# Optimization experiments

Hardware: AMD Instinct MI355X
Metric: run time of the kernel (lower is better)

Reference implementation:

```python
import jax, jax.numpy as jnp
import numpy as np

N, E, IN, ED, H, C, G, NC = 50000, 800000, 128, 32, 4, 16, 64, 2
HC = H * C  # 64
NEG_SLOPE = 0.2
EPS = 1e-5


def _layernorm(x, g, b):
    mu = jnp.mean(x, axis=-1, keepdims=True)
    var = jnp.mean((x - mu) ** 2, axis=-1, keepdims=True)
    return (x - mu) * jax.lax.rsqrt(var + EPS) * g + b


def _gat(x, src, dst, edge_attr, W, a_src, a_dst, We, a_edge, b):
    """PyG GATConv (v1) with edge features, concat=True."""
    n = x.shape[0]
    h, c = a_src.shape
    xw = (x @ W).reshape(n, h, c)                       # [N,H,C]
    al_src = jnp.sum(xw * a_src, axis=-1)               # [N,H]
    al_dst = jnp.sum(xw * a_dst, axis=-1)               # [N,H]
    ew = (edge_attr @ We).reshape(-1, h, c)             # [Ef,H,C]
    al_e = jnp.sum(ew * a_edge, axis=-1)                # [Ef,H]
    alpha = al_src[src] + al_dst[dst] + al_e            # [Ef,H]
    alpha = jnp.where(alpha > 0, alpha, NEG_SLOPE * alpha)
    # segment softmax over incoming edges of each dst node
    amax = jax.ops.segment_max(alpha, dst, num_segments=n)
    amax = jnp.where(jnp.isfinite(amax), amax, 0.0)
    ex = jnp.exp(alpha - amax[dst])
    denom = jax.ops.segment_sum(ex, dst, num_segments=n)
    att = ex / (denom[dst] + 1e-16)                     # [Ef,H]
    msg = xw[src] * att[:, :, None]                     # [Ef,H,C]
    out = jax.ops.segment_sum(msg, dst, num_segments=n) # [N,H,C]
    return out.reshape(n, h * c) + b


def setup_inputs() -> dict:
    ks = jax.random.split(jax.random.key(0), 24)
    s = 0.1
    inp = {
        "x": jax.random.normal(ks[0], (N, IN), jnp.float32),
        "edge_attr": jax.random.normal(ks[1], (E, ED), jnp.float32),
        "W1": jax.random.normal(ks[2], (IN, HC), jnp.float32) * s,
        "as1": jax.random.normal(ks[3], (H, C), jnp.float32) * s,
        "ad1": jax.random.normal(ks[4], (H, C), jnp.float32) * s,
        "We1": jax.random.normal(ks[5], (ED, HC), jnp.float32) * s,
        "ae1": jax.random.normal(ks[6], (H, C), jnp.float32) * s,
        "b1": jnp.zeros((HC,), jnp.float32),
        "W2": jax.random.normal(ks[7], (HC, HC), jnp.float32) * s,
        "as2": jax.random.normal(ks[8], (H, C), jnp.float32) * s,
        "ad2": jax.random.normal(ks[9], (H, C), jnp.float32) * s,
        "We2": jax.random.normal(ks[10], (ED, HC), jnp.float32) * s,
        "ae2": jax.random.normal(ks[11], (H, C), jnp.float32) * s,
        "b2": jnp.zeros((HC,), jnp.float32),
        "g1": jnp.ones((HC,), jnp.float32),
        "be1": jnp.zeros((HC,), jnp.float32),
        "fw1": jax.random.normal(ks[12], (HC, 32), jnp.float32) * s,
        "fb1": jnp.zeros((32,), jnp.float32),
        "g2": jnp.ones((32,), jnp.float32),
        "be2": jnp.zeros((32,), jnp.float32),
        "fw2": jax.random.normal(ks[13], (32, NC), jnp.float32) * s,
        "fb2": jnp.zeros((NC,), jnp.float32),
        "edge_index": jax.random.randint(ks[14], (2, E), 0, N, jnp.int64),
        "batch": jnp.sort(jax.random.randint(ks[15], (N,), 0, G, jnp.int64)),
    }
    return inp


def reference(x, edge_attr, W1, as1, ad1, We1, ae1, b1, W2, as2, ad2, We2, ae2,
              b2, g1, be1, fw1, fb1, g2, be2, fw2, fb2, edge_index, batch):
    src, dst = edge_index[0], edge_index[1]
    e = edge_attr.shape[0]
    # add_self_loops with fill_value='mean' (mean of incoming edge_attr per node)
    cnt = jax.ops.segment_sum(jnp.ones((e,), x.dtype), dst, num_segments=N)
    loop_ea = jax.ops.segment_sum(edge_attr, dst, num_segments=N) / jnp.clip(cnt, 1.0)[:, None]
    ar = jnp.arange(N)
    src_f = jnp.concatenate([src, ar])
    dst_f = jnp.concatenate([dst, ar])
    ea_f = jnp.concatenate([edge_attr, loop_ea], axis=0)

    h = _gat(x, src_f, dst_f, ea_f, W1, as1, ad1, We1, ae1, b1)
    h = jax.nn.relu(h)
    h = _layernorm(h, g1, be1)
    h = _gat(h, src_f, dst_f, ea_f, W2, as2, ad2, We2, ae2, b2)
    h = jax.nn.relu(h)
    pooled = jax.ops.segment_max(h, batch, num_segments=G)   # global_max_pool
    pooled = jnp.where(jnp.isfinite(pooled), pooled, 0.0)
    z = pooled @ fw1 + fb1
    z = _layernorm(z, g2, be2)
    z = jax.nn.relu(z)
    # dropout(p=0.4) is identity in eval mode
    z = z @ fw2 + fb2
    return jax.nn.log_softmax(z, axis=1)
```

## Files before the change

kernel.cpp:

```cpp
#include <hip/hip_runtime.h>
#include <math.h>

#define N_NODES 50000
#define N_EDGES 800000
#define IN_DIM 128
#define ED_DIM 32
#define NH 4
#define CH 16
#define HC 64
#define NG 64
#define NCL 2
#define NEG_SLOPE 0.2f
#define LN_EPS 1e-5f
#define NBLK1 196
#define NB_TILE 3125
#define NB_ECH 3125

__global__ void k_scan_local(const int* __restrict__ cnt, int* __restrict__ tmp_ex,
                             int* __restrict__ bsum) {
    __shared__ int sd[256];
    int t = threadIdx.x, idx = blockIdx.x * 256 + t;
    int v = (idx < N_NODES) ? cnt[idx] : 0;
    sd[t] = v; __syncthreads();
    for (int off = 1; off < 256; off <<= 1) {
        int add = (t >= off) ? sd[t - off] : 0;
        __syncthreads();
        sd[t] += add;
        __syncthreads();
    }
    if (idx < N_NODES) tmp_ex[idx] = sd[t] - v;
    if (t == 255) bsum[blockIdx.x] = sd[t];
}

__global__ __launch_bounds__(256) void k_phase1(
        const float* __restrict__ X, const float* __restrict__ W,
        const float* __restrict__ AS, const float* __restrict__ AD,
        float* __restrict__ XW, float* __restrict__ ALS, float* __restrict__ ALD,
        const float* __restrict__ ea,
        const float* __restrict__ We1, const float* __restrict__ ae1,
        const float* __restrict__ We2, const float* __restrict__ ae2,
        float4* __restrict__ ale8,
        const int* __restrict__ dst, int* __restrict__ cnt, int* __restrict__ rank_e) {
    __shared__ float smem[IN_DIM * HC + 16 * IN_DIM];
    int job = blockIdx.x % 3;
    int bid = blockIdx.x / 3;
    int t = threadIdx.x;
    if (job == 0) {
        const int K = IN_DIM;
        float* sW = smem;
        float* sX = smem + K * HC;
        for (int i = t; i < K * HC; i += 256) sW[i] = W[i];
        int nb = bid * 16;
        for (int i = t; i < 16 * K; i += 256) sX[i] = X[(long long)nb * K + i];
        __syncthreads();
        int sub = t >> 6, j = t & 63;
        float acc[4] = {0.f, 0.f, 0.f, 0.f};
        #pragma unroll 8
        for (int k = 0; k < K; ++k) {
            float wv = sW[k * HC + j];
            #pragma unroll
            for (int q = 0; q < 4; ++q) acc[q] += sX[(sub + 4 * q) * K + k] * wv;
        }
        float as_ = AS[j], ad_ = AD[j];
        #pragma unroll
        for (int q = 0; q < 4; ++q) {
            int n = nb + sub + 4 * q;
            XW[(long long)n * HC + j] = acc[q];
            float vs = acc[q] * as_, vd = acc[q] * ad_;
            #pragma unroll
            for (int m = 1; m < 16; m <<= 1) { vs += __shfl_xor(vs, m); vd += __shfl_xor(vd, m); }
            if ((j & 15) == 0) {
                int h = j >> 4;
                ALS[n * 4 + h] = vs; ALD[n * 4 + h] = vd;
            }
        }
    } else if (job == 1) {
        float* sVe = smem;
        {
            int d = t >> 3, k = t & 7;
            int l = k >> 2, h = k & 3;
            const float* We = l ? We2 : We1;
            const float* ae = l ? ae2 : ae1;
            float s = 0.f;
            #pragma unroll
            for (int c = 0; c < CH; ++c) s += We[d * HC + h * CH + c] * ae[h * CH + c];
            sVe[d * 8 + k] = s;
        }
        __syncthreads();
        int e = bid * 256 + t;
        if (e >= N_EDGES) return;
        float a[8];
        #pragma unroll
        for (int k = 0; k < 8; ++k) a[k] = 0.f;
        const float4* er4 = (const float4*)(ea + (long long)e * ED_DIM);
        #pragma unroll
        for (int q = 0; q < ED_DIM / 4; ++q) {
            float4 v = er4[q];
            float ev[4] = {v.x, v.y, v.z, v.w};
            #pragma unroll
            for (int u = 0; u < 4; ++u) {
                #pragma unroll
                for (int k = 0; k < 8; ++k) a[k] += ev[u] * sVe[(q * 4 + u) * 8 + k];
            }
        }
        float4* out = ale8 + (long long)e * 2;
        out[0] = make_float4(a[0], a[1], a[2], a[3]);
        out[1] = make_float4(a[4], a[5], a[6], a[7]);
    } else {
        int e = bid * 256 + t;
        if (e < N_EDGES) rank_e[e] = atomicAdd(&cnt[dst[e]], 1);
    }
}

__global__ void k_scan_perm(const int* __restrict__ tmp_ex, const int* __restrict__ bsum,
                            int* __restrict__ row_start,
                            const int* __restrict__ dst, const int* __restrict__ srcI,
                            const int* __restrict__ rank_e, int2* __restrict__ perm_src) {
    __shared__ int sd[256];
    __shared__ int sboff[256];
    int t = threadIdx.x;
    int v = (t < NBLK1) ? bsum[t] : 0;
    sd[t] = v; __syncthreads();
    for (int off = 1; off < 256; off <<= 1) {
        int add = (t >= off) ? sd[t - off] : 0;
        __syncthreads();
        sd[t] += add;
        __syncthreads();
    }
    sboff[t] = sd[t] - v;
    __syncthreads();
    if (blockIdx.x < NBLK1) {
        int idx = blockIdx.x * 256 + t;
        if (idx < N_NODES) row_start[idx] = tmp_ex[idx] + sboff[blockIdx.x];
        if (idx == 0) row_start[N_NODES] = N_EDGES;
    } else {
        int e = (blockIdx.x - NBLK1) * 256 + t;
        if (e < N_EDGES) {
            int d = dst[e];
            int pos = tmp_ex[d] + sboff[d >> 8] + rank_e[e];
            perm_src[pos] = make_int2(e, srcI[e]);
        }
    }
}

__global__ void k_agg1x(const int* __restrict__ rs, const int2* __restrict__ ps,
                        const float* __restrict__ ale8,
                        const float* __restrict__ ALS, const float* __restrict__ ALD,
                        const float* __restrict__ XW, const float* __restrict__ bias,
                        const float* __restrict__ gam, const float* __restrict__ bet,
                        const float* __restrict__ W2,
                        const float* __restrict__ AS2, const float* __restrict__ AD2,
                        float* __restrict__ XW2, float* __restrict__ ALS2,
                        float* __restrict__ ALD2) {
    __shared__ float sh[4][HC];
    int wid = threadIdx.x >> 6;
    int n = (blockIdx.x * blockDim.x + threadIdx.x) >> 6;
    if (n >= N_NODES) return;
    int lane = threadIdx.x & 63;
    int h = lane >> 4;
    int e0 = rs[n], e1 = rs[n + 1];
    float adn = ALD[n * 4 + h];
    float acc0 = 0.f, l0 = 0.f, as0 = 0.f;
    float acc1 = 0.f, l1 = 0.f, as1 = 0.f;
    float acc2 = 0.f, l2 = 0.f, as2 = 0.f;
    float acc3 = 0.f, l3 = 0.f, as3 = 0.f;
    int e = e0;
    for (; e + 3 < e1; e += 4) {
        int2 pA = ps[e], pB = ps[e + 1], pC = ps[e + 2], pD = ps[e + 3];
        float aeA = ale8[(long long)pA.x * 8 + h];
        float aeB = ale8[(long long)pB.x * 8 + h];
        float aeC = ale8[(long long)pC.x * 8 + h];
        float aeD = ale8[(long long)pD.x * 8 + h];
        float xA = XW[pA.y * HC + lane];
        float xB = XW[pB.y * HC + lane];
        float xC = XW[pC.y * HC + lane];
        float xD = XW[pD.y * HC + lane];
        float aA = ALS[pA.y * 4 + h] + adn + aeA;
        float aB = ALS[pB.y * 4 + h] + adn + aeB;
        float aC = ALS[pC.y * 4 + h] + adn + aeC;
        float aD = ALS[pD.y * 4 + h] + adn + aeD;
        aA = aA > 0.f ? aA : NEG_SLOPE * aA;
        aB = aB > 0.f ? aB : NEG_SLOPE * aB;
        aC = aC > 0.f ? aC : NEG_SLOPE * aC;
        aD = aD > 0.f ? aD : NEG_SLOPE * aD;
        float qA = __expf(aA), qB = __expf(aB), qC = __expf(aC), qD = __expf(aD);
        acc0 += qA * xA; l0 += qA; as0 += aeA;
        acc1 += qB * xB; l1 += qB; as1 += aeB;
        acc2 += qC * xC; l2 += qC; as2 += aeC;
        acc3 += qD * xD; l3 += qD; as3 += aeD;
    }
    for (; e < e1; ++e) {
        int2 pA = ps[e];
        float aeA = ale8[(long long)pA.x * 8 + h];
        float xA = XW[pA.y * HC + lane];
        float aA = ALS[pA.y * 4 + h] + adn + aeA;
        aA = aA > 0.f ? aA : NEG_SLOPE * aA;
        float qA = __expf(aA);
        acc0 += qA * xA; l0 += qA; as0 += aeA;
    }
    int d = e1 - e0;
    float invd = 1.f / (float)(d > 0 ? d : 1);
    float aSelf = ALS[n * 4 + h] + adn + (as0 + as1 + as2 + as3) * invd;
    aSelf = aSelf > 0.f ? aSelf : NEG_SLOPE * aSelf;
    float pS = __expf(aSelf);
    float acc = (acc0 + acc1) + (acc2 + acc3) + pS * XW[n * HC + lane];
    float l = (l0 + l1) + (l2 + l3) + pS;
    float v = acc / (l + 1e-16f) + bias[lane];
    v = fmaxf(v, 0.f);
    {
        float s1 = v;
        #pragma unroll
        for (int mm = 1; mm < 64; mm <<= 1) s1 += __shfl_xor(s1, mm);
        float mean = s1 * (1.f / 64.f);
        float dd = v - mean;
        float s2 = dd * dd;
        #pragma unroll
        for (int mm = 1; mm < 64; mm <<= 1) s2 += __shfl_xor(s2, mm);
        float var = s2 * (1.f / 64.f);
        v = dd * rsqrtf(var + LN_EPS) * gam[lane] + bet[lane];
    }
    sh[wid][lane] = v;
    __syncthreads();
    float a2 = 0.f;
    #pragma unroll 8
    for (int k = 0; k < HC; ++k) {
        a2 += sh[wid][k] * W2[k * HC + lane];
    }
    XW2[(long long)n * HC + lane] = a2;
    float vs = a2 * AS2[lane], vd = a2 * AD2[lane];
    #pragma unroll
    for (int m = 1; m < 16; m <<= 1) { vs += __shfl_xor(vs, m); vd += __shfl_xor(vd, m); }
    if ((lane & 15) == 0) {
        ALS2[n * 4 + h] = vs; ALD2[n * 4 + h] = vd;
    }
}

__global__ void k_agg2p(const int* __restrict__ rs, const int2* __restrict__ ps,
                        const float* __restrict__ ale8,
                        const float* __restrict__ ALS, const float* __restrict__ ALD,
                        const float* __restrict__ XW, const float* __restrict__ bias,
                        const int* __restrict__ batch, float* __restrict__ pooled) {
    int n = (blockIdx.x * blockDim.x + threadIdx.x) >> 6;
    if (n >= N_NODES) return;
    int lane = threadIdx.x & 63;
    int h = lane >> 4;
    int e0 = rs[n], e1 = rs[n + 1];
    float adn = ALD[n * 4 + h];
    float acc0 = 0.f, l0 = 0.f, as0 = 0.f;
    float acc1 = 0.f, l1 = 0.f, as1 = 0.f;
    float acc2 = 0.f, l2 = 0.f, as2 = 0.f;
    float acc3 = 0.f, l3 = 0.f, as3 = 0.f;
    int e = e0;
    for (; e + 3 < e1; e += 4) {
        int2 pA = ps[e], pB = ps[e + 1], pC = ps[e + 2], pD = ps[e + 3];
        float aeA = ale8[(long long)pA.x * 8 + 4 + h];
        float aeB = ale8[(long long)pB.x * 8 + 4 + h];
        float aeC = ale8[(long long)pC.x * 8 + 4 + h];
        float aeD = ale8[(long long)pD.x * 8 + 4 + h];
        float xA = XW[pA.y * HC + lane];
        float xB = XW[pB.y * HC + lane];
        float xC = XW[pC.y * HC + lane];
        float xD = XW[pD.y * HC + lane];
        float aA = ALS[pA.y * 4 + h] + adn + aeA;
        float aB = ALS[pB.y * 4 + h] + adn + aeB;
        float aC = ALS[pC.y * 4 + h] + adn + aeC;
        float aD = ALS[pD.y * 4 + h] + adn + aeD;
        aA = aA > 0.f ? aA : NEG_SLOPE * aA;
        aB = aB > 0.f ? aB : NEG_SLOPE * aB;
        aC = aC > 0.f ? aC : NEG_SLOPE * aC;
        aD = aD > 0.f ? aD : NEG_SLOPE * aD;
        float qA = __expf(aA), qB = __expf(aB), qC = __expf(aC), qD = __expf(aD);
        acc0 += qA * xA; l0 += qA; as0 += aeA;
        acc1 += qB * xB; l1 += qB; as1 += aeB;
        acc2 += qC * xC; l2 += qC; as2 += aeC;
        acc3 += qD * xD; l3 += qD; as3 += aeD;
    }
    for (; e < e1; ++e) {
        int2 pA = ps[e];
        float aeA = ale8[(long long)pA.x * 8 + 4 + h];
        float xA = XW[pA.y * HC + lane];
        float aA = ALS[pA.y * 4 + h] + adn + aeA;
        aA = aA > 0.f ? aA : NEG_SLOPE * aA;
        float qA = __expf(aA);
        acc0 += qA * xA; l0 += qA; as0 += aeA;
    }
    int d = e1 - e0;
    float invd = 1.f / (float)(d > 0 ? d : 1);
    float aSelf = ALS[n * 4 + h] + adn + (as0 + as1 + as2 + as3) * invd;
    aSelf = aSelf > 0.f ? aSelf : NEG_SLOPE * aSelf;
    float pS = __expf(aSelf);
    float acc = (acc0 + acc1) + (acc2 + acc3) + pS * XW[n * HC + lane];
    float l = (l0 + l1) + (l2 + l3) + pS;
    float v = acc / (l + 1e-16f) + bias[lane];
    v = fmaxf(v, 0.f);
    int g = batch[n];
    atomicMax((unsigned int*)&pooled[g * HC + lane], __float_as_uint(v));
}

__global__ void k_head(const float* __restrict__ pooled,
                       const float* __restrict__ fw1, const float* __restrict__ fb1,
                       const float* __restrict__ g2, const float* __restrict__ be2,
                       const float* __restrict__ fw2, const float* __restrict__ fb2,
                       float* __restrict__ out) {
    int g = blockIdx.x;
    int j = threadIdx.x;
    float z = 0.f;
    if (j < 32) {
        for (int k = 0; k < HC; ++k) z += pooled[g * HC + k] * fw1[k * 32 + j];
        z += fb1[j];
    }
    float s1 = (j < 32) ? z : 0.f;
    for (int m = 1; m < 32; m <<= 1) s1 += __shfl_xor(s1, m, 32);
    float mean = s1 * (1.f / 32.f);
    float d = z - mean;
    float s2 = (j < 32) ? d * d : 0.f;
    for (int m = 1; m < 32; m <<= 1) s2 += __shfl_xor(s2, m, 32);
    float var = s2 * (1.f / 32.f);
    float zz = 0.f;
    if (j < 32) {
        zz = d * rsqrtf(var + LN_EPS) * g2[j] + be2[j];
        zz = fmaxf(zz, 0.f);
    }
    float p0 = (j < 32) ? zz * fw2[j * NCL + 0] : 0.f;
    float p1 = (j < 32) ? zz * fw2[j * NCL + 1] : 0.f;
    for (int m = 1; m < 32; m <<= 1) { p0 += __shfl_xor(p0, m, 32); p1 += __shfl_xor(p1, m, 32); }
    if (j == 0) {
        float l0 = p0 + fb2[0], l1 = p1 + fb2[1];
        float mx = fmaxf(l0, l1);
        float ls = mx + logf(__expf(l0 - mx) + __expf(l1 - mx));
        out[g * NCL + 0] = l0 - ls;
        out[g * NCL + 1] = l1 - ls;
    }
}

extern "C" void kernel_launch(void* const* d_in, const int* in_sizes, int n_in,
                              void* d_out, int out_size, void* d_ws, size_t ws_size,
                              hipStream_t stream) {
    const float* x   = (const float*)d_in[0];
    const float* ea  = (const float*)d_in[1];
    const float* W1  = (const float*)d_in[2];
    const float* as1 = (const float*)d_in[3];
    const float* ad1 = (const float*)d_in[4];
    const float* We1 = (const float*)d_in[5];
    const float* ae1 = (const float*)d_in[6];
    const float* b1  = (const float*)d_in[7];
    const float* W2  = (const float*)d_in[8];
    const float* as2 = (const float*)d_in[9];
    const float* ad2 = (const float*)d_in[10];
    const float* We2 = (const float*)d_in[11];
    const float* ae2 = (const float*)d_in[12];
    const float* b2  = (const float*)d_in[13];
    const float* g1  = (const float*)d_in[14];
    const float* be1 = (const float*)d_in[15];
    const float* fw1 = (const float*)d_in[16];
    const float* fb1 = (const float*)d_in[17];
    const float* g2  = (const float*)d_in[18];
    const float* be2 = (const float*)d_in[19];
    const float* fw2 = (const float*)d_in[20];
    const float* fb2 = (const float*)d_in[21];
    const int* eidx  = (const int*)d_in[22];
    const int* batch = (const int*)d_in[23];
    const int* srcI = eidx;
    const int* dstI = eidx + N_EDGES;

    char* w = (char*)d_ws;
    auto alloc = [&](size_t bytes) { char* p = w; w += (bytes + 255) & ~(size_t)255; return p; };
    int*   cnt       = (int*)  alloc((size_t)N_NODES * 4);
    int*   row_start = (int*)  alloc((size_t)(N_NODES + 1) * 4);
    int*   rank_e    = (int*)  alloc((size_t)N_EDGES * 4);
    int*   tmp_ex    = (int*)  alloc((size_t)N_NODES * 4);
    int*   bsum      = (int*)  alloc(256 * 4);
    int2*  perm_src  = (int2*) alloc((size_t)N_EDGES * 8);
    float4* ale8     = (float4*)alloc((size_t)N_EDGES * 32);
    float* xw1       = (float*)alloc((size_t)N_NODES * HC * 4);
    float* als1      = (float*)alloc((size_t)N_NODES * 4 * 4);
    float* ald1      = (float*)alloc((size_t)N_NODES * 4 * 4);
    float* xw2       = (float*)alloc((size_t)N_NODES * HC * 4);
    float* als2      = (float*)alloc((size_t)N_NODES * 4 * 4);
    float* ald2      = (float*)alloc((size_t)N_NODES * 4 * 4);
    float* pooled    = (float*)alloc((size_t)NG * HC * 4);

    hipMemsetAsync(cnt, 0, (size_t)N_NODES * 4, stream);
    hipMemsetAsync(pooled, 0, (size_t)NG * HC * 4, stream);

    k_phase1<<<3 * NB_TILE, 256, 0, stream>>>(x, W1, as1, ad1, xw1, als1, ald1,
                                              ea, We1, ae1, We2, ae2, ale8,
                                              dstI, cnt, rank_e);
    k_scan_local<<<NBLK1, 256, 0, stream>>>(cnt, tmp_ex, bsum);
    k_scan_perm<<<NBLK1 + NB_ECH, 256, 0, stream>>>(tmp_ex, bsum, row_start,
                                                    dstI, srcI, rank_e, perm_src);

    k_agg1x<<<N_NODES / 4, 256, 0, stream>>>(row_start, perm_src, (const float*)ale8,
                                             als1, ald1, xw1, b1, g1, be1,
                                             W2, as2, ad2, xw2, als2, ald2);
    k_agg2p<<<N_NODES / 4, 256, 0, stream>>>(row_start, perm_src, (const float*)ale8,
                                             als2, ald2, xw2, b2, batch, pooled);

    k_head<<<NG, 64, 0, stream>>>(pooled, fw1, fb1, g2, be2, fw2, fb2, (float*)d_out);
}
```

Measured before the change: 435.4 us.

## Reschedule stages: histogram first, fuse scan/perm with projection, split layer-2 matmul

The edge histogram now runs as its own kernel first. The layer-1 projection, edge attention coefficients, CSR row_start and edge permutation are merged into one k_mid launch, so the scan/perm work overlaps with the dense compute. The layer-2 matmul moves out of the aggregation kernel into a separate tiled k_xw kernel, which writes an intermediate h1 buffer. The pooled max in the layer-2 aggregation is pre-reduced within each block for warps that share a graph, cutting global atomics. This trades one extra launch and an extra round trip of h1 through memory for better matmul reuse and less atomic contention.

```diff
diff --git a/kernel.cpp b/kernel.cpp
--- a/kernel.cpp
+++ b/kernel.cpp
@@ -14,7 +14,12 @@
 #define LN_EPS 1e-5f
 #define NBLK1 196
 #define NB_TILE 3125
-#define NB_ECH 3125
+
+__global__ void k_hist(const int* __restrict__ dst, int* __restrict__ cnt,
+                       int* __restrict__ rank_e) {
+    int e = blockIdx.x * 256 + threadIdx.x;
+    if (e < N_EDGES) rank_e[e] = atomicAdd(&cnt[dst[e]], 1);
+}
 
 __global__ void k_scan_local(const int* __restrict__ cnt, int* __restrict__ tmp_ex,
                              int* __restrict__ bsum) {
@@ -32,7 +37,7 @@
     if (t == 255) bsum[blockIdx.x] = sd[t];
 }
 
-__global__ __launch_bounds__(256) void k_phase1(
+__global__ __launch_bounds__(256) void k_mid(
         const float* __restrict__ X, const float* __restrict__ W,
         const float* __restrict__ AS, const float* __restrict__ AD,
         float* __restrict__ XW, float* __restrict__ ALS, float* __restrict__ ALD,
@@ -40,120 +45,154 @@
         const float* __restrict__ We1, const float* __restrict__ ae1,
         const float* __restrict__ We2, const float* __restrict__ ae2,
         float4* __restrict__ ale8,
-        const int* __restrict__ dst, int* __restrict__ cnt, int* __restrict__ rank_e) {
+        const int* __restrict__ tmp_ex, const int* __restrict__ bsum,
+        int* __restrict__ row_start,
+        const int* __restrict__ dst, const int* __restrict__ srcI,
+        const int* __restrict__ rank_e, int2* __restrict__ perm_src) {
     __shared__ float smem[IN_DIM * HC + 16 * IN_DIM];
-    int job = blockIdx.x % 3;
-    int bid = blockIdx.x / 3;
+    int b = blockIdx.x;
     int t = threadIdx.x;
-    if (job == 0) {
-        const int K = IN_DIM;
-        float* sW = smem;
-        float* sX = smem + K * HC;
-        for (int i = t; i < K * HC; i += 256) sW[i] = W[i];
-        int nb = bid * 16;
-        for (int i = t; i < 16 * K; i += 256) sX[i] = X[(long long)nb * K + i];
-        __syncthreads();
-        int sub = t >> 6, j = t & 63;
-        float acc[4] = {0.f, 0.f, 0.f, 0.f};
-        #pragma unroll 8
-        for (int k = 0; k < K; ++k) {
-            float wv = sW[k * HC + j];
+    if (b < 3 * NB_TILE) {
+        int job = b % 3;
+        int bid = b / 3;
+        if (job == 0) {
+            const int K = IN_DIM;
+            float* sW = smem;
+            float* sX = smem + K * HC;
+            for (int i = t; i < K * HC; i += 256) sW[i] = W[i];
+            int nb = bid * 16;
+            for (int i = t; i < 16 * K; i += 256) sX[i] = X[(long long)nb * K + i];
+            __syncthreads();
+            int sub = t >> 6, j = t & 63;
+            float acc[4] = {0.f, 0.f, 0.f, 0.f};
+            #pragma unroll 8
+            for (int k = 0; k < K; ++k) {
+                float wv = sW[k * HC + j];
+                #pragma unroll
+                for (int q = 0; q < 4; ++q) acc[q] += sX[(sub + 4 * q) * K + k] * wv;
+            }
+            float as_ = AS[j], ad_ = AD[j];
             #pragma unroll
-            for (int q = 0; q < 4; ++q) acc[q] += sX[(sub + 4 * q) * K + k] * wv;
-        }
-        float as_ = AS[j], ad_ = AD[j];
-        #pragma unroll
-        for (int q = 0; q < 4; ++q) {
-            int n = nb + sub + 4 * q;
-            XW[(long long)n * HC + j] = acc[q];
-            float vs = acc[q] * as_, vd = acc[q] * ad_;
+            for (int q = 0; q < 4; ++q) {
+                int n = nb + sub + 4 * q;
+                XW[(long long)n * HC + j] = acc[q];
+                float vs = acc[q] * as_, vd = acc[q] * ad_;
+                #pragma unroll
+                for (int m = 1; m < 16; m <<= 1) { vs += __shfl_xor(vs, m); vd += __shfl_xor(vd, m); }
+                if ((j & 15) == 0) {
+                    int h = j >> 4;
+                    ALS[n * 4 + h] = vs; ALD[n * 4 + h] = vd;
+                }
+            }
+        } else if (job == 1) {
+            float* sVe = smem;
+            {
+                int d = t >> 3, k = t & 7;
+                int l = k >> 2, h = k & 3;
+                const float* We = l ? We2 : We1;
+                const float* ae = l ? ae2 : ae1;
+                float s = 0.f;
+                #pragma unroll
+                for (int c = 0; c < CH; ++c) s += We[d * HC + h * CH + c] * ae[h * CH + c];
+                sVe[d * 8 + k] = s;
+            }
+            __syncthreads();
+            int e = bid * 256 + t;
+            float a[8];
             #pragma unroll
-            for (int m = 1; m < 16; m <<= 1) { vs += __shfl_xor(vs, m); vd += __shfl_xor(vd, m); }
-            if ((j & 15) == 0) {
-                int h = j >> 4;
-                ALS[n * 4 + h] = vs; ALD[n * 4 + h] = vd;
+            for (int k = 0; k < 8; ++k) a[k] = 0.f;
+            const float4* er4 = (const float4*)(ea + (long long)e * ED_DIM);
+            #pragma unroll
+            for (int q = 0; q < ED_DIM / 4; ++q) {
+                float4 v = er4[q];
+                float ev[4] = {v.x, v.y, v.z, v.w};
+                #pragma unroll
+                for (int u = 0; u < 4; ++u) {
+                    #pragma unroll
+                    for (int k = 0; k < 8; ++k) a[k] += ev[u] * sVe[(q * 4 + u) * 8 + k];
+                }
             }
-        }
-    } else if (job == 1) {
-        float* sVe = smem;
-        {
-            int d = t >> 3, k = t & 7;
-            int l = k >> 2, h = k & 3;
-            const float* We = l ? We2 : We1;
-            const float* ae = l ? ae2 : ae1;
-            float s = 0.f;
-            #pragma unroll
-            for (int c = 0; c < CH; ++c) s += We[d * HC + h * CH + c] * ae[h * CH + c];
-            sVe[d * 8 + k] = s;
-        }
-        __syncthreads();
-        int e = bid * 256 + t;
-        if (e >= N_EDGES) return;
-        float a[8];
-        #pragma unroll
-        for (int k = 0; k < 8; ++k) a[k] = 0.f;
-        const float4* er4 = (const float4*)(ea + (long long)e * ED_DIM);
-        #pragma unroll
-        for (int q = 0; q < ED_DIM / 4; ++q) {
-            float4 v = er4[q];
-            float ev[4] = {v.x, v.y, v.z, v.w};
-            #pragma unroll
-            for (int u = 0; u < 4; ++u) {
-                #pragma unroll
-                for (int k = 0; k < 8; ++k) a[k] += ev[u] * sVe[(q * 4 + u) * 8 + k];
+            float4* out = ale8 + (long long)e * 2;
+            out[0] = make_float4(a[0], a[1], a[2], a[3]);
+            out[1] = make_float4(a[4], a[5], a[6], a[7]);
+        } else {
+            int* sd = (int*)smem;
+            int* sboff = sd + 256;
+            int v = (t < NBLK1) ? bsum[t] : 0;
+            sd[t] = v; __syncthreads();
+            for (int off = 1; off < 256; off <<= 1) {
+                int add = (t >= off) ? sd[t - off] : 0;
+                __syncthreads();
+                sd[t] += add;
+                __syncthreads();
             }
-        }
-        float4* out = ale8 + (long long)e * 2;
-        out[0] = make_float4(a[0], a[1], a[2], a[3]);
-        out[1] = make_float4(a[4], a[5], a[6], a[7]);
-    } else {
-        int e = bid * 256 + t;
-        if (e < N_EDGES) rank_e[e] = atomicAdd(&cnt[dst[e]], 1);
-    }
-}
-
-__global__ void k_scan_perm(const int* __restrict__ tmp_ex, const int* __restrict__ bsum,
-                            int* __restrict__ row_start,
-                            const int* __restrict__ dst, const int* __restrict__ srcI,
-                            const int* __restrict__ rank_e, int2* __restrict__ perm_src) {
-    __shared__ int sd[256];
-    __shared__ int sboff[256];
-    int t = threadIdx.x;
-    int v = (t < NBLK1) ? bsum[t] : 0;
-    sd[t] = v; __syncthreads();
-    for (int off = 1; off < 256; off <<= 1) {
-        int add = (t >= off) ? sd[t - off] : 0;
-        __syncthreads();
-        sd[t] += add;
-        __syncthreads();
-    }
-    sboff[t] = sd[t] - v;
-    __syncthreads();
-    if (blockIdx.x < NBLK1) {
-        int idx = blockIdx.x * 256 + t;
-        if (idx < N_NODES) row_start[idx] = tmp_ex[idx] + sboff[blockIdx.x];
-        if (idx == 0) row_start[N_NODES] = N_EDGES;
-    } else {
-        int e = (blockIdx.x - NBLK1) * 256 + t;
-        if (e < N_EDGES) {
+            sboff[t] = sd[t] - v;
+            __syncthreads();
+            int e = bid * 256 + t;
             int d = dst[e];
             int pos = tmp_ex[d] + sboff[d >> 8] + rank_e[e];
             perm_src[pos] = make_int2(e, srcI[e]);
         }
-    }
-}
-
-__global__ void k_agg1x(const int* __restrict__ rs, const int2* __restrict__ ps,
-                        const float* __restrict__ ale8,
-                        const float* __restrict__ ALS, const float* __restrict__ ALD,
-                        const float* __restrict__ XW, const float* __restrict__ bias,
-                        const float* __restrict__ gam, const float* __restrict__ bet,
-                        const float* __restrict__ W2,
-                        const float* __restrict__ AS2, const float* __restrict__ AD2,
-                        float* __restrict__ XW2, float* __restrict__ ALS2,
-                        float* __restrict__ ALD2) {
-    __shared__ float sh[4][HC];
-    int wid = threadIdx.x >> 6;
+    } else {
+        int bid = b - 3 * NB_TILE;
+        int* sd = (int*)smem;
+        int* sboff = sd + 256;
+        int v = (t < NBLK1) ? bsum[t] : 0;
+        sd[t] = v; __syncthreads();
+        for (int off = 1; off < 256; off <<= 1) {
+            int add = (t >= off) ? sd[t - off] : 0;
+            __syncthreads();
+            sd[t] += add;
+            __syncthreads();
+        }
+        sboff[t] = sd[t] - v;
+        __syncthreads();
+        int idx = bid * 256 + t;
+        if (idx < N_NODES) row_start[idx] = tmp_ex[idx] + sboff[bid];
+        if (idx == 0) row_start[N_NODES] = N_EDGES;
+    }
+}
+
+template<int K>
+__global__ void k_xw(const float* __restrict__ X, const float* __restrict__ W,
+                     const float* __restrict__ AS, const float* __restrict__ AD,
+                     float* __restrict__ XW, float* __restrict__ ALS, float* __restrict__ ALD) {
+    __shared__ float sW[K * HC];
+    __shared__ float sX[16 * K];
+    int t = threadIdx.x;
+    for (int i = t; i < K * HC; i += 256) sW[i] = W[i];
+    int nb = blockIdx.x * 16;
+    for (int i = t; i < 16 * K; i += 256) sX[i] = X[(long long)nb * K + i];
+    __syncthreads();
+    int sub = t >> 6, j = t & 63;
+    float acc[4] = {0.f, 0.f, 0.f, 0.f};
+    #pragma unroll 8
+    for (int k = 0; k < K; ++k) {
+        float wv = sW[k * HC + j];
+        #pragma unroll
+        for (int q = 0; q < 4; ++q) acc[q] += sX[(sub + 4 * q) * K + k] * wv;
+    }
+    float as_ = AS[j], ad_ = AD[j];
+    #pragma unroll
+    for (int q = 0; q < 4; ++q) {
+        int n = nb + sub + 4 * q;
+        XW[(long long)n * HC + j] = acc[q];
+        float vs = acc[q] * as_, vd = acc[q] * ad_;
+        #pragma unroll
+        for (int m = 1; m < 16; m <<= 1) { vs += __shfl_xor(vs, m); vd += __shfl_xor(vd, m); }
+        if ((j & 15) == 0) {
+            int h = j >> 4;
+            ALS[n * 4 + h] = vs; ALD[n * 4 + h] = vd;
+        }
+    }
+}
+
+__global__ void k_agg1(const int* __restrict__ rs, const int2* __restrict__ ps,
+                       const float* __restrict__ ale8,
+                       const float* __restrict__ ALS, const float* __restrict__ ALD,
+                       const float* __restrict__ XW, const float* __restrict__ bias,
+                       const float* __restrict__ gam, const float* __restrict__ bet,
+                       float* __restrict__ OUT) {
     int n = (blockIdx.x * blockDim.x + threadIdx.x) >> 6;
     if (n >= N_NODES) return;
     int lane = threadIdx.x & 63;
@@ -219,29 +258,18 @@
         float var = s2 * (1.f / 64.f);
         v = dd * rsqrtf(var + LN_EPS) * gam[lane] + bet[lane];
     }
-    sh[wid][lane] = v;
-    __syncthreads();
-    float a2 = 0.f;
-    #pragma unroll 8
-    for (int k = 0; k < HC; ++k) {
-        a2 += sh[wid][k] * W2[k * HC + lane];
-    }
-    XW2[(long long)n * HC + lane] = a2;
-    float vs = a2 * AS2[lane], vd = a2 * AD2[lane];
-    #pragma unroll
-    for (int m = 1; m < 16; m <<= 1) { vs += __shfl_xor(vs, m); vd += __shfl_xor(vd, m); }
-    if ((lane & 15) == 0) {
-        ALS2[n * 4 + h] = vs; ALD2[n * 4 + h] = vd;
-    }
-}
-
-__global__ void k_agg2p(const int* __restrict__ rs, const int2* __restrict__ ps,
+    OUT[(long long)n * HC + lane] = v;
+}
+
+__global__ void k_agg2r(const int* __restrict__ rs, const int2* __restrict__ ps,
                         const float* __restrict__ ale8,
                         const float* __restrict__ ALS, const float* __restrict__ ALD,
                         const float* __restrict__ XW, const float* __restrict__ bias,
                         const int* __restrict__ batch, float* __restrict__ pooled) {
-    int n = (blockIdx.x * blockDim.x + threadIdx.x) >> 6;
-    if (n >= N_NODES) return;
+    __shared__ float sv[4][HC];
+    __shared__ int sgp[4];
+    int wid = threadIdx.x >> 6;
+    int n = blockIdx.x * 4 + wid;
     int lane = threadIdx.x & 63;
     int h = lane >> 4;
     int e0 = rs[n], e1 = rs[n + 1];
@@ -293,8 +321,21 @@
     float l = (l0 + l1) + (l2 + l3) + pS;
     float v = acc / (l + 1e-16f) + bias[lane];
     v = fmaxf(v, 0.f);
-    int g = batch[n];
-    atomicMax((unsigned int*)&pooled[g * HC + lane], __float_as_uint(v));
+    sv[wid][lane] = v;
+    if (lane == 0) sgp[wid] = batch[n];
+    __syncthreads();
+    int g = sgp[wid];
+    float m = v;
+    bool leader = true;
+    #pragma unroll
+    for (int w2 = 0; w2 < 4; ++w2) {
+        if (w2 == wid) continue;
+        if (sgp[w2] == g) {
+            if (w2 < wid) leader = false;
+            else m = fmaxf(m, sv[w2][lane]);
+        }
+    }
+    if (leader) atomicMax((unsigned int*)&pooled[g * HC + lane], __float_as_uint(m));
 }
 
 __global__ void k_head(const float* __restrict__ pooled,
@@ -375,25 +416,26 @@
     float* xw1       = (float*)alloc((size_t)N_NODES * HC * 4);
     float* als1      = (float*)alloc((size_t)N_NODES * 4 * 4);
     float* ald1      = (float*)alloc((size_t)N_NODES * 4 * 4);
-    float* xw2       = (float*)alloc((size_t)N_NODES * HC * 4);
+    float* h1        = (float*)alloc((size_t)N_NODES * HC * 4);
     float* als2      = (float*)alloc((size_t)N_NODES * 4 * 4);
     float* ald2      = (float*)alloc((size_t)N_NODES * 4 * 4);
     float* pooled    = (float*)alloc((size_t)NG * HC * 4);
+    float* xw2 = xw1;
 
     hipMemsetAsync(cnt, 0, (size_t)N_NODES * 4, stream);
     hipMemsetAsync(pooled, 0, (size_t)NG * HC * 4, stream);
 
-    k_phase1<<<3 * NB_TILE, 256, 0, stream>>>(x, W1, as1, ad1, xw1, als1, ald1,
-                                              ea, We1, ae1, We2, ae2, ale8,
-                                              dstI, cnt, rank_e);
+    k_hist<<<NB_TILE, 256, 0, stream>>>(dstI, cnt, rank_e);
     k_scan_local<<<NBLK1, 256, 0, stream>>>(cnt, tmp_ex, bsum);
-    k_scan_perm<<<NBLK1 + NB_ECH, 256, 0, stream>>>(tmp_ex, bsum, row_start,
-                                                    dstI, srcI, rank_e, perm_src);
-
-    k_agg1x<<<N_NODES / 4, 256, 0, stream>>>(row_start, perm_src, (const float*)ale8,
-                                             als1, ald1, xw1, b1, g1, be1,
-                                             W2, as2, ad2, xw2, als2, ald2);
-    k_agg2p<<<N_NODES / 4, 256, 0, stream>>>(row_start, perm_src, (const float*)ale8,
+    k_mid<<<3 * NB_TILE + NBLK1, 256, 0, stream>>>(x, W1, as1, ad1, xw1, als1, ald1,
+                                                   ea, We1, ae1, We2, ae2, ale8,
+                                                   tmp_ex, bsum, row_start,
+                                                   dstI, srcI, rank_e, perm_src);
+
+    k_agg1<<<N_NODES / 4, 256, 0, stream>>>(row_start, perm_src, (const float*)ale8,
+                                            als1, ald1, xw1, b1, g1, be1, h1);
+    k_xw<HC><<<NB_TILE, 256, 0, stream>>>(h1, W2, as2, ad2, xw2, als2, ald2);
+    k_agg2r<<<N_NODES / 4, 256, 0, stream>>>(row_start, perm_src, (const float*)ale8,
                                              als2, ald2, xw2, b2, batch, pooled);
 
     k_head<<<NG, 64, 0, stream>>>(pooled, fw1, fb1, g2, be2, fw2, fb2, (float*)d_out);
```

New measurement: 431.5 us. No clear change (-0.9%).
